# Optimization experiments

Measured on AMD Instinct MI355X. Metric: run time of the kernel, lower is better.

Reference implementation:

```python
import jax, jax.numpy as jnp
import numpy as np

D_MODEL = 1024
NUM_HEADS = 16
HEAD_DIM = D_MODEL // NUM_HEADS


def setup_inputs() -> dict:
    key = jax.random.key(0)
    ks = jax.random.split(key, 9)
    s = 1.0 / np.sqrt(D_MODEL)
    x = jax.random.normal(ks[0], (2, 2048, D_MODEL), dtype=jnp.float32)
    Wq = jax.random.uniform(ks[1], (D_MODEL, D_MODEL), jnp.float32, -s, s)
    bq = jax.random.uniform(ks[2], (D_MODEL,), jnp.float32, -s, s)
    Wk = jax.random.uniform(ks[3], (D_MODEL, D_MODEL), jnp.float32, -s, s)
    bk = jax.random.uniform(ks[4], (D_MODEL,), jnp.float32, -s, s)
    Wv = jax.random.uniform(ks[5], (D_MODEL, D_MODEL), jnp.float32, -s, s)
    bv = jax.random.uniform(ks[6], (D_MODEL,), jnp.float32, -s, s)
    Wo = jax.random.uniform(ks[7], (D_MODEL, D_MODEL), jnp.float32, -s, s)
    bo = jax.random.uniform(ks[8], (D_MODEL,), jnp.float32, -s, s)
    return {"x": x, "Wq": Wq, "bq": bq, "Wk": Wk, "bk": bk,
            "Wv": Wv, "bv": bv, "Wo": Wo, "bo": bo}


def reference(x, Wq, bq, Wk, bk, Wv, bv, Wo, bo):
    B, S, D = x.shape
    H, Hd = NUM_HEADS, HEAD_DIM
    # projections (torch Linear: x @ W.T + b; here W stored as [in, out])
    q = (x @ Wq + bq).reshape(B, S, H, Hd).transpose(0, 2, 1, 3)  # [B,H,S,Hd]
    k = (x @ Wk + bk).reshape(B, S, H, Hd).transpose(0, 2, 1, 3)
    v = (x @ Wv + bv).reshape(B, S, H, Hd).transpose(0, 2, 1, 3)
    scale = 1.0 / jnp.sqrt(jnp.asarray(Hd, dtype=x.dtype))
    scores = jnp.einsum('bhqd,bhkd->bhqk', q, k) * scale  # [B,H,S,S]
    attn = jax.nn.softmax(scores, axis=-1)
    out = jnp.einsum('bhqk,bhkd->bhqd', attn, v)  # [B,H,S,Hd]
    out = out.transpose(0, 2, 1, 3).reshape(B, S, D)
    return out @ Wo + bo
```

## Files before the change

### kernel.cpp

```cpp
#include <hip/hip_runtime.h>
#include <hip/hip_bf16.h>
#include <string.h>


#define DM 1024
#define S_LEN 2048
#define NH 16
#define HD 64

using u16 = unsigned short;
using u32 = unsigned int;

typedef short bf16x8 __attribute__((ext_vector_type(8)));
typedef float f32x4  __attribute__((ext_vector_type(4)));
typedef float f32x16 __attribute__((ext_vector_type(16)));
typedef unsigned int u32x2 __attribute__((ext_vector_type(2)));

__device__ __forceinline__ u16 f2bf(float f) {
    u32 i = __float_as_uint(f);
    u32 r = i + 0x7fffu + ((i >> 16) & 1u);
    return (u16)(r >> 16);
}
__device__ __forceinline__ u32 pk_bf16(float a, float b) {
    __hip_bfloat162 h = __float22bfloat162_rn(float2{a, b});
    u32 r; memcpy(&r, &h, 4);
    return r;
}

__global__ __launch_bounds__(256) void prep_x(const float* __restrict__ X, u16* __restrict__ out) {
    int i = (blockIdx.x * 256 + threadIdx.x) * 4;
    float4 v = *(const float4*)(X + i);
    *(uint2*)(out + i) = make_uint2(pk_bf16(v.x, v.y), pk_bf16(v.z, v.w));
}

__global__ __launch_bounds__(256) void prep_wt3(
    const float* __restrict__ W0, const float* __restrict__ W1, const float* __restrict__ W2,
    u16* __restrict__ T0, u16* __restrict__ T1, u16* __restrict__ T2)
{
    __shared__ u16 tile[64][72];
    const float* W = (blockIdx.z == 0) ? W0 : (blockIdx.z == 1) ? W1 : W2;
    u16* WT        = (blockIdx.z == 0) ? T0 : (blockIdx.z == 1) ? T1 : T2;
    const int t = threadIdx.x;
    const int n0 = blockIdx.x * 64, k0 = blockIdx.y * 64;
    #pragma unroll
    for (int it = 0; it < 4; it++) {
        int k = it * 16 + (t >> 4);
        int n = (t & 15) * 4;
        float4 v = *(const float4*)(W + (size_t)(k0 + k) * DM + n0 + n);
        tile[n + 0][k] = f2bf(v.x);
        tile[n + 1][k] = f2bf(v.y);
        tile[n + 2][k] = f2bf(v.z);
        tile[n + 3][k] = f2bf(v.w);
    }
    __syncthreads();
    int n = t >> 2, kg = (t & 3) * 16;
    uint4 a = *(const uint4*)&tile[n][kg];
    uint4 b = *(const uint4*)&tile[n][kg + 8];
    *(uint4*)(WT + (size_t)(n0 + n) * DM + k0 + kg)     = a;
    *(uint4*)(WT + (size_t)(n0 + n) * DM + k0 + kg + 8) = b;
}

__global__ __launch_bounds__(256) void prep_wt1(const float* __restrict__ W, u16* __restrict__ WT) {
    __shared__ u16 tile[64][72];
    const int t = threadIdx.x;
    const int n0 = blockIdx.x * 64, k0 = blockIdx.y * 64;
    #pragma unroll
    for (int it = 0; it < 4; it++) {
        int k = it * 16 + (t >> 4);
        int n = (t & 15) * 4;
        float4 v = *(const float4*)(W + (size_t)(k0 + k) * DM + n0 + n);
        tile[n + 0][k] = f2bf(v.x);
        tile[n + 1][k] = f2bf(v.y);
        tile[n + 2][k] = f2bf(v.z);
        tile[n + 3][k] = f2bf(v.w);
    }
    __syncthreads();
    int n = t >> 2, kg = (t & 3) * 16;
    uint4 a = *(const uint4*)&tile[n][kg];
    uint4 b = *(const uint4*)&tile[n][kg + 8];
    *(uint4*)(WT + (size_t)(n0 + n) * DM + k0 + kg)     = a;
    *(uint4*)(WT + (size_t)(n0 + n) * DM + k0 + kg + 8) = b;
}

__global__ __launch_bounds__(256, 3) void gemm_qkv_z(
    const u16* __restrict__ WQT, const u16* __restrict__ WKT, const u16* __restrict__ WVT,
    const u16* __restrict__ X,
    const float* __restrict__ bq, const float* __restrict__ bk, const float* __restrict__ bv,
    u16* __restrict__ outQ, u16* __restrict__ outK, u16* __restrict__ outVT)
{
    __shared__ u16 Ws[128][72];
    __shared__ u16 Xs[128][72];

    const int z = blockIdx.z;
    const u16* WT = (z == 0) ? WQT : (z == 1) ? WKT : WVT;

    const int t = threadIdx.x;
    const int w = t >> 6, lane = t & 63, quad = lane >> 4, l16 = lane & 15;
    const int Mb0 = blockIdx.x * 128;
    const int Nb0 = blockIdx.y * 128;
    const int mloc = (w & 1) * 64, nloc = (w >> 1) * 64;

    f32x4 acc[4][4];
    #pragma unroll
    for (int i = 0; i < 4; i++)
        #pragma unroll
        for (int j = 0; j < 4; j++) acc[i][j] = (f32x4){0.f, 0.f, 0.f, 0.f};

    const int sr = t >> 3, sc8 = (t & 7) * 8;

    for (int k0 = 0; k0 < DM; k0 += 64) {
        __syncthreads();
        #pragma unroll
        for (int i = 0; i < 4; i++) {
            int r = i * 32 + sr;
            *(uint4*)&Ws[r][sc8] = *(const uint4*)(WT + (size_t)(Mb0 + r) * DM + k0 + sc8);
            *(uint4*)&Xs[r][sc8] = *(const uint4*)(X  + (size_t)(Nb0 + r) * DM + k0 + sc8);
        }
        __syncthreads();

        #pragma unroll
        for (int ks = 0; ks < 2; ks++) {
            const int kk = ks * 32 + quad * 8;
            bf16x8 af[4], bf[4];
            #pragma unroll
            for (int mt = 0; mt < 4; mt++)
                af[mt] = *(const bf16x8*)&Ws[mloc + mt * 16 + l16][kk];
            #pragma unroll
            for (int nt = 0; nt < 4; nt++)
                bf[nt] = *(const bf16x8*)&Xs[nloc + nt * 16 + l16][kk];
            #pragma unroll
            for (int mt = 0; mt < 4; mt++)
                #pragma unroll
                for (int nt = 0; nt < 4; nt++)
                    acc[mt][nt] = __builtin_amdgcn_mfma_f32_16x16x32_bf16(af[mt], bf[nt], acc[mt][nt], 0, 0, 0);
        }
    }

    const float QS = 0.18033688f;
    if (z <= 1) {
        u16* outP = (z == 0) ? outQ : outK;
        const float* bias = (z == 0) ? bq : bk;
        const float scale = (z == 0) ? QS : 1.0f;
        #pragma unroll
        for (int mt = 0; mt < 4; mt++) {
            int nf0 = Mb0 + mloc + mt * 16 + quad * 4;
            int hh = nf0 >> 6, hd = nf0 & 63;
            float4 bb = *(const float4*)(bias + nf0);
            #pragma unroll
            for (int nt = 0; nt < 4; nt++) {
                int m = Nb0 + nloc + nt * 16 + l16;
                int b = m >> 11, s = m & 2047;
                size_t idx = (size_t)(b * NH + hh) * 131072 + (size_t)s * 64 + hd;
                *(uint2*)(outP + idx) = make_uint2(
                    pk_bf16((acc[mt][nt][0] + bb.x) * scale, (acc[mt][nt][1] + bb.y) * scale),
                    pk_bf16((acc[mt][nt][2] + bb.z) * scale, (acc[mt][nt][3] + bb.w) * scale));
            }
        }
    } else {
        #pragma unroll
        for (int mt = 0; mt < 4; mt++) {
            #pragma unroll
            for (int r = 0; r < 4; r++) {
                int nf = Mb0 + mloc + mt * 16 + quad * 4 + r;
                int hh = nf >> 6, hd = nf & 63;
                float bb = bv[nf];
                #pragma unroll
                for (int nt = 0; nt < 4; nt++) {
                    int m = Nb0 + nloc + nt * 16 + l16;
                    int b = m >> 11, s = m & 2047;
                    outVT[(size_t)(b * NH + hh) * 131072 + (size_t)hd * S_LEN + s]
                        = f2bf(acc[mt][nt][r] + bb);
                }
            }
        }
    }
}

__global__ __launch_bounds__(256) void gemm_out(
    const u16* __restrict__ A, const u16* __restrict__ B,
    const float* __restrict__ bias, float* __restrict__ of32)
{
    __shared__ u16 As[64][72];
    __shared__ u16 Bs[128][72];

    const int t = threadIdx.x;
    const int w = t >> 6, lane = t & 63, quad = lane >> 4, l16 = lane & 15;
    const int Mb0 = blockIdx.x * 64;
    const int Nb0 = blockIdx.y * 128;
    const int Mb = Mb0 + (w & 1) * 32;
    const int Nb = Nb0 + (w >> 1) * 64;
    const int mloc = (w & 1) * 32, nloc = (w >> 1) * 64;

    f32x4 acc[2][4];
    #pragma unroll
    for (int i = 0; i < 2; i++)
        #pragma unroll
        for (int j = 0; j < 4; j++) acc[i][j] = (f32x4){0.f, 0.f, 0.f, 0.f};

    const int sr = t >> 3, sc8 = (t & 7) * 8;

    for (int k0 = 0; k0 < DM; k0 += 64) {
        const int h = k0 >> 6;
        __syncthreads();
        #pragma unroll
        for (int i = 0; i < 2; i++) {
            int r = i * 32 + sr;
            *(uint4*)&As[r][sc8] = *(const uint4*)(A + (size_t)(Mb0 + r) * DM + k0 + sc8);
        }
        #pragma unroll
        for (int i = 0; i < 4; i++) {
            int r = i * 32 + sr;
            int m = Nb0 + r;
            int b = m >> 11, s = m & 2047;
            *(uint4*)&Bs[r][sc8] =
                *(const uint4*)(B + (size_t)(b * NH + h) * 131072 + (size_t)s * 64 + sc8);
        }
        __syncthreads();

        #pragma unroll
        for (int ks = 0; ks < 2; ks++) {
            const int kk = ks * 32 + quad * 8;
            bf16x8 a0 = *(const bf16x8*)&As[mloc + l16][kk];
            bf16x8 a1 = *(const bf16x8*)&As[mloc + 16 + l16][kk];
            #pragma unroll
            for (int nt = 0; nt < 4; nt++) {
                bf16x8 bf = *(const bf16x8*)&Bs[nloc + nt * 16 + l16][kk];
                acc[0][nt] = __builtin_amdgcn_mfma_f32_16x16x32_bf16(a0, bf, acc[0][nt], 0, 0, 0);
                acc[1][nt] = __builtin_amdgcn_mfma_f32_16x16x32_bf16(a1, bf, acc[1][nt], 0, 0, 0);
            }
        }
    }
    #pragma unroll
    for (int mt = 0; mt < 2; mt++) {
        int nf0 = Mb + mt * 16 + quad * 4;
        float4 bvv = *(const float4*)(bias + nf0);
        #pragma unroll
        for (int nt = 0; nt < 4; nt++) {
            int m = Nb + nt * 16 + l16;
            float4 o;
            o.x = acc[mt][nt][0] + bvv.x; o.y = acc[mt][nt][1] + bvv.y;
            o.z = acc[mt][nt][2] + bvv.z; o.w = acc[mt][nt][3] + bvv.w;
            *(float4*)(of32 + (size_t)m * DM + nf0) = o;
        }
    }
}

__global__ __launch_bounds__(512, 4) void attn_mfma(
    const u16* __restrict__ Q, const u16* __restrict__ K, const u16* __restrict__ VT,
    u16* __restrict__ O)
{
    __shared__ __align__(64) u16 smem[2][2][2][64][72];

    const int t = threadIdx.x;
    const int w = t >> 6, lane = t & 63;
    const int wq = w & 3, half = w >> 2;
    const int l32 = lane & 31, h = lane >> 5;
    const int bh = blockIdx.y;
    const int q0 = blockIdx.x * 128;
    const size_t base = (size_t)bh * 131072;

    const int qrow = q0 + wq * 32 + l32;
    bf16x8 qf[4];
    #pragma unroll
    for (int ks = 0; ks < 4; ks++)
        qf[ks] = *(const bf16x8*)(Q + base + (size_t)qrow * 64 + ks * 16 + h * 8);

    const short onebf = (short)0x3F80;
    const bf16x8 ones = {onebf, onebf, onebf, onebf, onebf, onebf, onebf, onebf};

    f32x16 o[2], lacc;
    #pragma unroll
    for (int ht = 0; ht < 2; ht++)
        #pragma unroll
        for (int i = 0; i < 16; i++) o[ht][i] = 0.f;
    #pragma unroll
    for (int i = 0; i < 16; i++) lacc[i] = 0.f;

    const int sr = t >> 3;
    const int sc8 = (t & 7) * 8;
    const u16* Kg = K + base;
    const u16* Vg = VT + base;

    *(uint4*)&smem[0][0][0][sr][sc8] = *(const uint4*)(Kg + (size_t)sr * 64 + sc8);
    *(uint4*)&smem[0][1][0][sr][sc8] = *(const uint4*)(Kg + (size_t)(16 * 64 + sr) * 64 + sc8);
    *(uint4*)&smem[1][0][0][sr][sc8] = *(const uint4*)(Vg + (size_t)sr * S_LEN + sc8);
    *(uint4*)&smem[1][1][0][sr][sc8] = *(const uint4*)(Vg + (size_t)sr * S_LEN + 16 * 64 + sc8);
    __syncthreads();

    for (int it = 0; it < 16; it++) {
        const int cur = it & 1;
        uint4 kra, krb, vra, vrb;
        if (it < 15) {
            kra = *(const uint4*)(Kg + (size_t)((it + 1) * 64 + sr) * 64 + sc8);
            krb = *(const uint4*)(Kg + (size_t)((it + 17) * 64 + sr) * 64 + sc8);
            vra = *(const uint4*)(Vg + (size_t)sr * S_LEN + (it + 1) * 64 + sc8);
            vrb = *(const uint4*)(Vg + (size_t)sr * S_LEN + (it + 17) * 64 + sc8);
        }

        const u16 (*Ksc)[72] = smem[0][half][cur];
        const u16 (*Vsc)[72] = smem[1][half][cur];

        #pragma unroll
        for (int kh = 0; kh < 2; kh++) {
            f32x16 s;
            #pragma unroll
            for (int i = 0; i < 16; i++) s[i] = 0.f;
            #pragma unroll
            for (int ks = 0; ks < 4; ks++) {
                bf16x8 kf = *(const bf16x8*)&Ksc[kh * 32 + l32][ks * 16 + h * 8];
                s = __builtin_amdgcn_mfma_f32_32x32x16_bf16(kf, qf[ks], s, 0, 0, 0);
            }
            float p[16];
            #pragma unroll
            for (int i = 0; i < 16; i++) p[i] = __builtin_amdgcn_exp2f(s[i]);
            u32 A0 = pk_bf16(p[0],  p[1]),  B0 = pk_bf16(p[2],  p[3]);
            u32 A1 = pk_bf16(p[4],  p[5]),  B1 = pk_bf16(p[6],  p[7]);
            u32 A2 = pk_bf16(p[8],  p[9]),  B2 = pk_bf16(p[10], p[11]);
            u32 A3 = pk_bf16(p[12], p[13]), B3 = pk_bf16(p[14], p[15]);
            u32x2 sA0 = __builtin_amdgcn_permlane32_swap(A0, A1, false, false);
            u32x2 sB0 = __builtin_amdgcn_permlane32_swap(B0, B1, false, false);
            u32x2 sA1 = __builtin_amdgcn_permlane32_swap(A2, A3, false, false);
            u32x2 sB1 = __builtin_amdgcn_permlane32_swap(B2, B3, false, false);
            union { bf16x8 v; u32 wd[4]; } fr0, fr1;
            fr0.wd[0] = sA0.x; fr0.wd[1] = sB0.x; fr0.wd[2] = sA0.y; fr0.wd[3] = sB0.y;
            fr1.wd[0] = sA1.x; fr1.wd[1] = sB1.x; fr1.wd[2] = sA1.y; fr1.wd[3] = sB1.y;

            lacc = __builtin_amdgcn_mfma_f32_32x32x16_bf16(fr0.v, ones, lacc, 0, 0, 0);
            lacc = __builtin_amdgcn_mfma_f32_32x32x16_bf16(fr1.v, ones, lacc, 0, 0, 0);

            #pragma unroll
            for (int ht = 0; ht < 2; ht++) {
                bf16x8 vf0 = *(const bf16x8*)&Vsc[ht * 32 + l32][kh * 32 + h * 8];
                o[ht] = __builtin_amdgcn_mfma_f32_32x32x16_bf16(fr0.v, vf0, o[ht], 0, 0, 0);
                bf16x8 vf1 = *(const bf16x8*)&Vsc[ht * 32 + l32][kh * 32 + 16 + h * 8];
                o[ht] = __builtin_amdgcn_mfma_f32_32x32x16_bf16(fr1.v, vf1, o[ht], 0, 0, 0);
            }
        }

        if (it < 15) {
            *(uint4*)&smem[0][0][cur ^ 1][sr][sc8] = kra;
            *(uint4*)&smem[0][1][cur ^ 1][sr][sc8] = krb;
            *(uint4*)&smem[1][0][cur ^ 1][sr][sc8] = vra;
            *(uint4*)&smem[1][1][cur ^ 1][sr][sc8] = vrb;
        }
        __syncthreads();
    }

    float* red = (float*)&smem[0][0][0][0][0];
    if (half) {
        #pragma unroll
        for (int i = 0; i < 16; i++) {
            red[((0 + wq) * 16 + i) * 64 + lane] = o[0][i];
            red[((4 + wq) * 16 + i) * 64 + lane] = o[1][i];
            red[((8 + wq) * 16 + i) * 64 + lane] = lacc[i];
        }
    }
    __syncthreads();
    if (!half) {
        #pragma unroll
        for (int i = 0; i < 16; i++) {
            o[0][i] += red[((0 + wq) * 16 + i) * 64 + lane];
            o[1][i] += red[((4 + wq) * 16 + i) * 64 + lane];
            lacc[i] += red[((8 + wq) * 16 + i) * 64 + lane];
        }
        float inv[16];
        #pragma unroll
        for (int r = 0; r < 16; r++) inv[r] = 1.0f / lacc[r];
        #pragma unroll
        for (int ht = 0; ht < 2; ht++)
            #pragma unroll
            for (int r = 0; r < 16; r++) {
                int q = q0 + wq * 32 + (r & 3) + 8 * (r >> 2) + 4 * h;
                O[base + (size_t)q * 64 + ht * 32 + l32] = f2bf(o[ht][r] * inv[r]);
            }
    }
}

extern "C" void kernel_launch(void* const* d_in, const int* in_sizes, int n_in,
                              void* d_out, int out_size, void* d_ws, size_t ws_size,
                              hipStream_t stream) {
    const float* x  = (const float*)d_in[0];
    const float* Wq = (const float*)d_in[1];
    const float* bq = (const float*)d_in[2];
    const float* Wk = (const float*)d_in[3];
    const float* bk = (const float*)d_in[4];
    const float* Wv = (const float*)d_in[5];
    const float* bv = (const float*)d_in[6];
    const float* Wo = (const float*)d_in[7];
    const float* bo = (const float*)d_in[8];
    float* out = (float*)d_out;

    u16* xbf = (u16*)d_out;
    u16* wqt = xbf + 4194304;
    u16* wkt = wqt + 1048576;
    u16* wvt = wkt + 1048576;

    u16* qws  = (u16*)d_ws;
    u16* kws  = qws + 4194304;
    u16* vtws = kws + 4194304;
    u16* wot  = kws;

    prep_x<<<4096, 256, 0, stream>>>(x, xbf);
    prep_wt3<<<dim3(16, 16, 3), 256, 0, stream>>>(Wq, Wk, Wv, wqt, wkt, wvt);

    gemm_qkv_z<<<dim3(8, 32, 3), 256, 0, stream>>>(wqt, wkt, wvt, xbf, bq, bk, bv,
                                                   qws, kws, vtws);

    attn_mfma<<<dim3(16, 32), 512, 0, stream>>>(qws, kws, vtws, qws);

    prep_wt1<<<dim3(16, 16), 256, 0, stream>>>(Wo, wot);
    gemm_out<<<dim3(16, 32), 256, 0, stream>>>(wot, qws, bo, out);
}
```

Measured before the change: 197.8 us.

## Double-buffer LDS tiles with register prefetch in QKV and output GEMMs

Both projection GEMMs now use two LDS buffers with a K-step of 32 instead of one buffer with a K-step of 64. The next tile's global loads are issued into registers before the current tile's MFMAs and written to the other buffer afterwards, so each iteration needs one barrier instead of two. The aim is to hide global memory latency behind compute. In exchange the loop runs twice as many iterations with fewer MFMAs between barriers, and the 36-element row pitch may change LDS bank-conflict behaviour.

```diff
diff --git a/kernel.cpp b/kernel.cpp
--- a/kernel.cpp
+++ b/kernel.cpp
@@ -88,8 +88,8 @@
     const float* __restrict__ bq, const float* __restrict__ bk, const float* __restrict__ bv,
     u16* __restrict__ outQ, u16* __restrict__ outK, u16* __restrict__ outVT)
 {
-    __shared__ u16 Ws[128][72];
-    __shared__ u16 Xs[128][72];
+    __shared__ u16 Ws[2][128][36];
+    __shared__ u16 Xs[2][128][36];
 
     const int z = blockIdx.z;
     const u16* WT = (z == 0) ? WQT : (z == 1) ? WKT : WVT;
@@ -106,34 +106,53 @@
         #pragma unroll
         for (int j = 0; j < 4; j++) acc[i][j] = (f32x4){0.f, 0.f, 0.f, 0.f};
 
-    const int sr = t >> 3, sc8 = (t & 7) * 8;
-
-    for (int k0 = 0; k0 < DM; k0 += 64) {
+    const int sr = t >> 2;
+    const int sc8 = (t & 3) * 8;
+
+    #pragma unroll
+    for (int i = 0; i < 2; i++) {
+        int r = i * 64 + sr;
+        *(uint4*)&Ws[0][r][sc8] = *(const uint4*)(WT + (size_t)(Mb0 + r) * DM + sc8);
+        *(uint4*)&Xs[0][r][sc8] = *(const uint4*)(X  + (size_t)(Nb0 + r) * DM + sc8);
+    }
+    __syncthreads();
+
+    for (int kt = 0; kt < 32; kt++) {
+        const int cur = kt & 1;
+        uint4 wr[2], xr[2];
+        if (kt < 31) {
+            const int k0 = (kt + 1) * 32;
+            #pragma unroll
+            for (int i = 0; i < 2; i++) {
+                int r = i * 64 + sr;
+                wr[i] = *(const uint4*)(WT + (size_t)(Mb0 + r) * DM + k0 + sc8);
+                xr[i] = *(const uint4*)(X  + (size_t)(Nb0 + r) * DM + k0 + sc8);
+            }
+        }
+
+        const int kk = quad * 8;
+        bf16x8 af[4], bf[4];
+        #pragma unroll
+        for (int mt = 0; mt < 4; mt++)
+            af[mt] = *(const bf16x8*)&Ws[cur][mloc + mt * 16 + l16][kk];
+        #pragma unroll
+        for (int nt = 0; nt < 4; nt++)
+            bf[nt] = *(const bf16x8*)&Xs[cur][nloc + nt * 16 + l16][kk];
+        #pragma unroll
+        for (int mt = 0; mt < 4; mt++)
+            #pragma unroll
+            for (int nt = 0; nt < 4; nt++)
+                acc[mt][nt] = __builtin_amdgcn_mfma_f32_16x16x32_bf16(af[mt], bf[nt], acc[mt][nt], 0, 0, 0);
+
+        if (kt < 31) {
+            #pragma unroll
+            for (int i = 0; i < 2; i++) {
+                int r = i * 64 + sr;
+                *(uint4*)&Ws[cur ^ 1][r][sc8] = wr[i];
+                *(uint4*)&Xs[cur ^ 1][r][sc8] = xr[i];
+            }
+        }
         __syncthreads();
-        #pragma unroll
-        for (int i = 0; i < 4; i++) {
-            int r = i * 32 + sr;
-            *(uint4*)&Ws[r][sc8] = *(const uint4*)(WT + (size_t)(Mb0 + r) * DM + k0 + sc8);
-            *(uint4*)&Xs[r][sc8] = *(const uint4*)(X  + (size_t)(Nb0 + r) * DM + k0 + sc8);
-        }
-        __syncthreads();
-
-        #pragma unroll
-        for (int ks = 0; ks < 2; ks++) {
-            const int kk = ks * 32 + quad * 8;
-            bf16x8 af[4], bf[4];
-            #pragma unroll
-            for (int mt = 0; mt < 4; mt++)
-                af[mt] = *(const bf16x8*)&Ws[mloc + mt * 16 + l16][kk];
-            #pragma unroll
-            for (int nt = 0; nt < 4; nt++)
-                bf[nt] = *(const bf16x8*)&Xs[nloc + nt * 16 + l16][kk];
-            #pragma unroll
-            for (int mt = 0; mt < 4; mt++)
-                #pragma unroll
-                for (int nt = 0; nt < 4; nt++)
-                    acc[mt][nt] = __builtin_amdgcn_mfma_f32_16x16x32_bf16(af[mt], bf[nt], acc[mt][nt], 0, 0, 0);
-        }
     }
 
     const float QS = 0.18033688f;
@@ -180,8 +199,8 @@
     const u16* __restrict__ A, const u16* __restrict__ B,
     const float* __restrict__ bias, float* __restrict__ of32)
 {
-    __shared__ u16 As[64][72];
-    __shared__ u16 Bs[128][72];
+    __shared__ u16 As[2][64][36];
+    __shared__ u16 Bs[2][128][36];
 
     const int t = threadIdx.x;
     const int w = t >> 6, lane = t & 63, quad = lane >> 4, l16 = lane & 15;
@@ -197,39 +216,58 @@
         #pragma unroll
         for (int j = 0; j < 4; j++) acc[i][j] = (f32x4){0.f, 0.f, 0.f, 0.f};
 
-    const int sr = t >> 3, sc8 = (t & 7) * 8;
-
-    for (int k0 = 0; k0 < DM; k0 += 64) {
-        const int h = k0 >> 6;
+    const int sr = t >> 2;
+    const int sc8 = (t & 3) * 8;
+
+    *(uint4*)&As[0][sr][sc8] = *(const uint4*)(A + (size_t)(Mb0 + sr) * DM + sc8);
+    #pragma unroll
+    for (int i = 0; i < 2; i++) {
+        int r = i * 64 + sr;
+        int m = Nb0 + r;
+        int b = m >> 11, s = m & 2047;
+        *(uint4*)&Bs[0][r][sc8] =
+            *(const uint4*)(B + (size_t)(b * NH + 0) * 131072 + (size_t)s * 64 + sc8);
+    }
+    __syncthreads();
+
+    for (int kt = 0; kt < 32; kt++) {
+        const int cur = kt & 1;
+        uint4 ar, br[2];
+        if (kt < 31) {
+            const int kn = kt + 1;
+            const int k0 = kn * 32;
+            const int hn = kn >> 1, cn = (kn & 1) * 32;
+            ar = *(const uint4*)(A + (size_t)(Mb0 + sr) * DM + k0 + sc8);
+            #pragma unroll
+            for (int i = 0; i < 2; i++) {
+                int r = i * 64 + sr;
+                int m = Nb0 + r;
+                int b = m >> 11, s = m & 2047;
+                br[i] = *(const uint4*)(B + (size_t)(b * NH + hn) * 131072 + (size_t)s * 64 + cn + sc8);
+            }
+        }
+
+        const int kk = quad * 8;
+        bf16x8 a0 = *(const bf16x8*)&As[cur][mloc + l16][kk];
+        bf16x8 a1 = *(const bf16x8*)&As[cur][mloc + 16 + l16][kk];
+        #pragma unroll
+        for (int nt = 0; nt < 4; nt++) {
+            bf16x8 bf = *(const bf16x8*)&Bs[cur][nloc + nt * 16 + l16][kk];
+            acc[0][nt] = __builtin_amdgcn_mfma_f32_16x16x32_bf16(a0, bf, acc[0][nt], 0, 0, 0);
+            acc[1][nt] = __builtin_amdgcn_mfma_f32_16x16x32_bf16(a1, bf, acc[1][nt], 0, 0, 0);
+        }
+
+        if (kt < 31) {
+            *(uint4*)&As[cur ^ 1][sr][sc8] = ar;
+            #pragma unroll
+            for (int i = 0; i < 2; i++) {
+                int r = i * 64 + sr;
+                *(uint4*)&Bs[cur ^ 1][r][sc8] = br[i];
+            }
+        }
         __syncthreads();
-        #pragma unroll
-        for (int i = 0; i < 2; i++) {
-            int r = i * 32 + sr;
-            *(uint4*)&As[r][sc8] = *(const uint4*)(A + (size_t)(Mb0 + r) * DM + k0 + sc8);
-        }
-        #pragma unroll
-        for (int i = 0; i < 4; i++) {
-            int r = i * 32 + sr;
-            int m = Nb0 + r;
-            int b = m >> 11, s = m & 2047;
-            *(uint4*)&Bs[r][sc8] =
-                *(const uint4*)(B + (size_t)(b * NH + h) * 131072 + (size_t)s * 64 + sc8);
-        }
-        __syncthreads();
-
-        #pragma unroll
-        for (int ks = 0; ks < 2; ks++) {
-            const int kk = ks * 32 + quad * 8;
-            bf16x8 a0 = *(const bf16x8*)&As[mloc + l16][kk];
-            bf16x8 a1 = *(const bf16x8*)&As[mloc + 16 + l16][kk];
-            #pragma unroll
-            for (int nt = 0; nt < 4; nt++) {
-                bf16x8 bf = *(const bf16x8*)&Bs[nloc + nt * 16 + l16][kk];
-                acc[0][nt] = __builtin_amdgcn_mfma_f32_16x16x32_bf16(a0, bf, acc[0][nt], 0, 0, 0);
-                acc[1][nt] = __builtin_amdgcn_mfma_f32_16x16x32_bf16(a1, bf, acc[1][nt], 0, 0, 0);
-            }
-        }
-    }
+    }
+
     #pragma unroll
     for (int mt = 0; mt < 2; mt++) {
         int nf0 = Mb + mt * 16 + quad * 4;
```

Measured after the change: 206.0 us. 1.04x slower.
